# Kernel optimization log

Measured on AMD Instinct MI355X. Metric: run time of the kernel, lower is better.

Reference implementation:

```python
import jax, jax.numpy as jnp
import numpy as np

B, C, H, W = 16, 256, 32, 32
NUM_LAYERS = 30
OUT = 16  # sqrt(out_channels)
EPS = 1e-5


def setup_inputs() -> dict:
    key = jax.random.key(0)
    k1, k2, k3 = jax.random.split(key, 3)
    x = jax.random.normal(k1, (B, C, H, W), dtype=jnp.float32)
    # delta_t ~ small positive values (module inits ~N(0.01, 0.005))
    delta_t = jax.random.uniform(k2, (NUM_LAYERS, 1), dtype=jnp.float32) * 0.02
    matrices = jax.random.normal(k3, (NUM_LAYERS, 1, 1, OUT, OUT), dtype=jnp.float32) * 0.1
    gamma = jnp.ones((H * W,), dtype=jnp.float32)   # BatchNorm2d weight, oc = i*i = H*W
    beta = jnp.zeros((H * W,), dtype=jnp.float32)   # BatchNorm2d bias
    return {"x": x, "delta_t": delta_t, "matrices": matrices, "gamma": gamma, "beta": beta}


def _bn_relu6(z, gamma, beta):
    # training-mode BatchNorm2d over channel axis 1 (channels = H*W), then ReLU6
    mean = jnp.mean(z, axis=(0, 2, 3), keepdims=True)
    var = jnp.mean(jnp.square(z - mean), axis=(0, 2, 3), keepdims=True)  # biased var
    zhat = (z - mean) * jax.lax.rsqrt(var + EPS)
    g = gamma.reshape(1, -1, 1, 1)
    b = beta.reshape(1, -1, 1, 1)
    return jnp.clip(zhat * g + b, 0.0, 6.0)


def reference(x, delta_t, matrices, gamma, beta):
    b, c, h, w = x.shape
    hw = h * w
    # feature_reshape: [B,C,H,W] -> [B,HW,C] -> [B,HW,out,out] (inn == out branch)
    x1 = x.reshape(b, c, hw).transpose(0, 2, 1).reshape(b, hw, OUT, OUT)
    dt = jnp.clip(delta_t, 0.0, 6.0)[:, 0]  # relu6(delta_t), shape [L]

    def step(y0, params):
        m, dtl = params  # m: [1,1,out,out] broadcasts elementwise against x1
        dydt = -y0 + _bn_relu6(y0 + m * x1, gamma, beta)
        return y0 + dtl * dydt, None

    y0, _ = jax.lax.scan(step, x1, (matrices, dt))
    # (y0 + x1): [B, HW, out, out] -> view [B,H,W,out*out] -> permute to [B,out*out,H,W]
    y = (y0 + x1).reshape(b, h, w, OUT * OUT).transpose(0, 3, 1, 2)
    return y
```

## Files before the change

kernel.cpp:

```cpp
#include <hip/hip_runtime.h>

typedef float v2f __attribute__((ext_vector_type(2)));
typedef float v4f __attribute__((ext_vector_type(4)));

#define HW      1024
#define NROWS   4096
#define NLAYERS 30
#define TPB     256

static __device__ __forceinline__ v2f pk_fma(v2f a, v2f b, v2f c) {
    v2f d; asm("v_pk_fma_f32 %0, %1, %2, %3" : "=v"(d) : "v"(a), "v"(b), "v"(c));
    return d;
}
static __device__ __forceinline__ v2f pk_add(v2f a, v2f b) {
    v2f d; asm("v_pk_add_f32 %0, %1, %2" : "=v"(d) : "v"(a), "v"(b));
    return d;
}

template <int CTRL, int RMASK>
__device__ __forceinline__ float dpp_add(float x) {
    int t = __builtin_amdgcn_update_dpp(0, __builtin_bit_cast(int, x),
                                        CTRL, RMASK, 0xf, true);
    return x + __builtin_bit_cast(float, t);
}
__device__ __forceinline__ float wave_sum64(float x) {
    x = dpp_add<0x111, 0xf>(x);
    x = dpp_add<0x112, 0xf>(x);
    x = dpp_add<0x114, 0xf>(x);
    x = dpp_add<0x118, 0xf>(x);
    x = dpp_add<0x142, 0xa>(x);
    x = dpp_add<0x143, 0xc>(x);
    return x;
}
__device__ __forceinline__ float bcast63(float x) {
    return __builtin_bit_cast(float,
        __builtin_amdgcn_readlane(__builtin_bit_cast(int, x), 63));
}

__global__ __launch_bounds__(TPB) void txp64(const float* __restrict__ src,
                                             float* __restrict__ dst,
                                             int M, int N) {
    __shared__ float tile[64][65];
    const int n0 = blockIdx.x * 64;
    const int m0 = blockIdx.y * 64;
    const int tx = threadIdx.x & 63;
    const int ty = threadIdx.x >> 6;
#pragma unroll
    for (int i = 0; i < 16; ++i) {
        const int r = ty + 4 * i;
        tile[r][tx] = src[(size_t)(m0 + r) * N + n0 + tx];
    }
    __syncthreads();
#pragma unroll
    for (int i = 0; i < 16; ++i) {
        const int r = ty + 4 * i;
        dst[(size_t)(n0 + r) * M + m0 + tx] = tile[tx][r];
    }
}

__global__ __launch_bounds__(64, 1) void ode_zreg(
    float* __restrict__ ws, const float* __restrict__ delta_t,
    const float* __restrict__ matrices, const float* __restrict__ gamma,
    const float* __restrict__ beta) {

    const int p    = blockIdx.x;
    const int lane = threadIdx.x;
    const int c0   = 4 * lane;
    float* row = ws + (size_t)p * NROWS;

    const float gp = gamma[p];
    const float bp = beta[p];

    v4f xr[16];
    v2f z[32];
    v2f s0 = {0.f, 0.f}, s1 = {0.f, 0.f}, q0 = {0.f, 0.f}, q1 = {0.f, 0.f};

    {
        const v4f m4 = *(const v4f*)(matrices + c0);
        const v2f mA = {m4.x, m4.y}, mB = {m4.z, m4.w};
#pragma unroll
        for (int j = 0; j < 16; ++j) {
            xr[j] = *(const v4f*)(row + 4 * lane + 256 * j);
            const v2f xA = {xr[j].x, xr[j].y}, xB = {xr[j].z, xr[j].w};
            z[2 * j]     = pk_fma(mA, xA, xA);
            z[2 * j + 1] = pk_fma(mB, xB, xB);
            s0 = pk_add(s0, z[2 * j]);
            q0 = pk_fma(z[2 * j], z[2 * j], q0);
            s1 = pk_add(s1, z[2 * j + 1]);
            q1 = pk_fma(z[2 * j + 1], z[2 * j + 1], q1);
        }
    }

    v4f   mqc = *(const v4f*)(matrices + c0);
    v4f   mqn = *(const v4f*)(matrices + 256 + c0);
    float dtc = delta_t[0];
    float dtn = delta_t[1];

    for (int k = 0; k < NLAYERS - 1; ++k) {
        asm volatile("" : "+v"(xr[0]), "+v"(xr[1]), "+v"(xr[2]), "+v"(xr[3]));
        asm volatile("" : "+v"(xr[4]), "+v"(xr[5]), "+v"(xr[6]), "+v"(xr[7]));
        asm volatile("" : "+v"(xr[8]), "+v"(xr[9]), "+v"(xr[10]), "+v"(xr[11]));
        asm volatile("" : "+v"(xr[12]), "+v"(xr[13]), "+v"(xr[14]), "+v"(xr[15]));

        const int k2 = (k + 2 < NLAYERS) ? k + 2 : NLAYERS - 1;
        const v4f   mq2   = *(const v4f*)(matrices + k2 * 256 + c0);
        const float dt_nn = delta_t[k2];

        const v2f sv = pk_add(s0, s1);
        const v2f qv = pk_add(q0, q1);
        const float S = bcast63(wave_sum64(sv.x + sv.y));
        const float Q = bcast63(wave_sum64(qv.x + qv.y));

        const float dtk  = __builtin_amdgcn_fmed3f(dtc, 0.0f, 6.0f);
        const float mean = S * (1.0f / 4096.0f);
        const float var  = fmaf(-mean, mean, Q * (1.0f / 4096.0f));
        const float rstd = rsqrtf(var + 1e-5f);
        const float g    = gp * rstd;
        const float b    = fmaf(-mean, g, bp);
        const float om   = 1.0f - dtk;
        const float gd   = g * dtk;
        const float bd   = b * dtk;
        const float hi   = 6.0f * dtk;
        const v2f gd2 = {gd, gd}, bd2 = {bd, bd};
        const v2f om2 = {om, om};
        const v2f omn = {-om, -om};
        const v2f mcA = {mqc.x, mqc.y}, mcB = {mqc.z, mqc.w};
        const v2f mnA = {mqn.x, mqn.y}, mnB = {mqn.z, mqn.w};
        const v2f dmA = pk_fma(omn, mcA, mnA);
        const v2f dmB = pk_fma(omn, mcB, mnB);

        s0 = (v2f){0.f, 0.f}; s1 = (v2f){0.f, 0.f};
        q0 = (v2f){0.f, 0.f}; q1 = (v2f){0.f, 0.f};

#pragma unroll
        for (int j = 0; j < 16; ++j) {
            const v2f xA = {xr[j].x, xr[j].y}, xB = {xr[j].z, xr[j].w};
            {
                const int e = 2 * j;
                v2f a = pk_fma(z[e], gd2, bd2);
                a.x = __builtin_amdgcn_fmed3f(a.x, 0.0f, hi);
                a.y = __builtin_amdgcn_fmed3f(a.y, 0.0f, hi);
                v2f u = pk_fma(dmA, xA, a);
                z[e] = pk_fma(om2, z[e], u);
                s0 = pk_add(s0, z[e]);
                q0 = pk_fma(z[e], z[e], q0);
            }
            {
                const int e = 2 * j + 1;
                v2f a = pk_fma(z[e], gd2, bd2);
                a.x = __builtin_amdgcn_fmed3f(a.x, 0.0f, hi);
                a.y = __builtin_amdgcn_fmed3f(a.y, 0.0f, hi);
                v2f u = pk_fma(dmB, xB, a);
                z[e] = pk_fma(om2, z[e], u);
                s1 = pk_add(s1, z[e]);
                q1 = pk_fma(z[e], z[e], q1);
            }
        }

        mqc = mqn; mqn = mq2; dtc = dtn; dtn = dt_nn;
    }

    {
        const v2f sv = pk_add(s0, s1);
        const v2f qv = pk_add(q0, q1);
        const float S = bcast63(wave_sum64(sv.x + sv.y));
        const float Q = bcast63(wave_sum64(qv.x + qv.y));

        const float dtk  = __builtin_amdgcn_fmed3f(dtc, 0.0f, 6.0f);
        const float mean = S * (1.0f / 4096.0f);
        const float var  = fmaf(-mean, mean, Q * (1.0f / 4096.0f));
        const float rstd = rsqrtf(var + 1e-5f);
        const float g    = gp * rstd;
        const float b    = fmaf(-mean, g, bp);
        const float om   = 1.0f - dtk;
        const float gd   = g * dtk;
        const float bd   = b * dtk;
        const float hi   = 6.0f * dtk;
        const v2f gd2 = {gd, gd}, bd2 = {bd, bd};
        const v2f om2 = {om, om};
        const v2f omn = {-om, -om};
        const v2f one2 = {1.0f, 1.0f};
        const v2f mcA = {mqc.x, mqc.y}, mcB = {mqc.z, mqc.w};
        const v2f dmA = pk_fma(omn, mcA, one2);
        const v2f dmB = pk_fma(omn, mcB, one2);

#pragma unroll
        for (int j = 0; j < 16; ++j) {
            const v2f xA = {xr[j].x, xr[j].y}, xB = {xr[j].z, xr[j].w};
            v2f o0, o1;
            {
                v2f a = pk_fma(z[2 * j], gd2, bd2);
                a.x = __builtin_amdgcn_fmed3f(a.x, 0.0f, hi);
                a.y = __builtin_amdgcn_fmed3f(a.y, 0.0f, hi);
                v2f u = pk_fma(dmA, xA, a);
                o0 = pk_fma(om2, z[2 * j], u);
            }
            {
                v2f a = pk_fma(z[2 * j + 1], gd2, bd2);
                a.x = __builtin_amdgcn_fmed3f(a.x, 0.0f, hi);
                a.y = __builtin_amdgcn_fmed3f(a.y, 0.0f, hi);
                v2f u = pk_fma(dmB, xB, a);
                o1 = pk_fma(om2, z[2 * j + 1], u);
            }
            v4f o4; o4.x = o0.x; o4.y = o0.y; o4.z = o1.x; o4.w = o1.y;
            *(v4f*)(row + 4 * lane + 256 * j) = o4;
        }
    }
}

__global__ __launch_bounds__(TPB) void ode_fused(const float* __restrict__ x,
                                                 const float* __restrict__ delta_t,
                                                 const float* __restrict__ matrices,
                                                 const float* __restrict__ gamma,
                                                 const float* __restrict__ beta,
                                                 float* __restrict__ out) {
    const int bid = blockIdx.x;
    const int p   = ((bid & 7) << 7) | (bid >> 3);
    const int t   = threadIdx.x;

    __shared__ float smat[(NLAYERS + 1) * 256];
    __shared__ float sdt[NLAYERS];
    __shared__ __align__(16) v2f red[2][4];

#pragma unroll
    for (int i = 0; i < NLAYERS; ++i)
        smat[i * 256 + t] = matrices[i * 256 + t];
    if (t < NLAYERS)
        sdt[t] = __builtin_amdgcn_fmed3f(delta_t[t], 0.0f, 6.0f);

    v2f x1[8], y[8];
#pragma unroll
    for (int k = 0; k < 8; ++k) {
        x1[k].x = x[(size_t)(t + 512 * k) * HW + p];
        x1[k].y = x[(size_t)(t + 512 * k + 256) * HW + p];
        y[k] = x1[k];
    }

    const float gp   = gamma[p];
    const float bp   = beta[p];
    const int   wid  = t >> 6;
    const int   lane = t & 63;

    __syncthreads();
    float m_cur = smat[t];

    for (int l = 0; l < NLAYERS; ++l) {
        const float dtl = sdt[l];
        const v2f m2    = {m_cur, m_cur};
        const v2f dt2   = {dtl, dtl};
        const v2f om2   = {1.0f - dtl, 1.0f - dtl};

        v2f z[8];
        v2f sA = {0.f, 0.f}, sB = {0.f, 0.f};
        v2f qA = {0.f, 0.f}, qB = {0.f, 0.f};
#pragma unroll
        for (int k = 0; k < 8; k += 2) {
            z[k]     = __builtin_elementwise_fma(m2, x1[k], y[k]);
            z[k + 1] = __builtin_elementwise_fma(m2, x1[k + 1], y[k + 1]);
            sA += z[k];
            sB += z[k + 1];
            qA = __builtin_elementwise_fma(z[k], z[k], qA);
            qB = __builtin_elementwise_fma(z[k + 1], z[k + 1], qB);
        }
#pragma unroll
        for (int k = 0; k < 8; ++k) y[k] *= om2;

        const v2f sv = sA + sB;
        const v2f qv = qA + qB;
        float s = wave_sum64(sv.x + sv.y);
        float q = wave_sum64(qv.x + qv.y);

        const int par = l & 1;
        if (lane == 63) { v2f w; w.x = s; w.y = q; red[par][wid] = w; }
        m_cur = smat[(l + 1) * 256 + t];
        __syncthreads();

        const float4 r0 = *(const float4*)&red[par][0];
        const float4 r1 = *(const float4*)&red[par][2];
        const float S  = (r0.x + r0.z) + (r1.x + r1.z);
        const float S2 = (r0.y + r0.w) + (r1.y + r1.w);

        const float mean = S * (1.0f / 4096.0f);
        const float var  = fmaf(-mean, mean, S2 * (1.0f / 4096.0f));
        const float rstd = rsqrtf(var + 1e-5f);
        const float g    = gp * rstd;
        const float bb   = fmaf(-mean, g, bp);
        const v2f g2 = {g, g}, b2 = {bb, bb};
        const v2f z0 = {0.f, 0.f}, s6 = {6.f, 6.f};
#pragma unroll
        for (int k = 0; k < 8; ++k) {
            v2f a = __builtin_elementwise_fma(z[k], g2, b2);
            a = __builtin_elementwise_max(a, z0);
            a = __builtin_elementwise_min(a, s6);
            y[k] = __builtin_elementwise_fma(dt2, a, y[k]);
        }
    }

#pragma unroll
    for (int k = 0; k < 8; ++k) {
        out[(size_t)(t + 512 * k) * HW + p]       = y[k].x + x1[k].x;
        out[(size_t)(t + 512 * k + 256) * HW + p] = y[k].y + x1[k].y;
    }
}

extern "C" void kernel_launch(void* const* d_in, const int* in_sizes, int n_in,
                              void* d_out, int out_size, void* d_ws, size_t ws_size,
                              hipStream_t stream) {
    const float* x        = (const float*)d_in[0];
    const float* delta_t  = (const float*)d_in[1];
    const float* matrices = (const float*)d_in[2];
    const float* gamma    = (const float*)d_in[3];
    const float* beta     = (const float*)d_in[4];
    float* out = (float*)d_out;

    const size_t need = (size_t)HW * NROWS * sizeof(float);
    if (d_ws != nullptr && ws_size >= need) {
        float* ws = (float*)d_ws;
        txp64<<<dim3(HW / 64, NROWS / 64), dim3(TPB), 0, stream>>>(x, ws, NROWS, HW);
        ode_zreg<<<dim3(HW), dim3(64), 0, stream>>>(ws, delta_t, matrices, gamma, beta);
        txp64<<<dim3(NROWS / 64, HW / 64), dim3(TPB), 0, stream>>>(ws, out, HW, NROWS);
    } else {
        ode_fused<<<dim3(HW), dim3(TPB), 0, stream>>>(x, delta_t, matrices, gamma, beta, out);
    }
}
```

Baseline: 111.5 us.

## Fuse transposes into single-wave ODE kernel with strided direct global access

Removes the two transpose kernels and the workspace round trip, so the single-wave-per-column ODE kernel reads x and writes out directly with stride-HW scalar accesses. Blocks are remapped so that neighbouring blocks touch nearby columns, which lets cache lines be shared through L2. This drops two launches and a full extra read and write of the tensor. In exchange, every load and store is an uncoalesced 4-byte access, and a lot more memory transactions are issued. The ode_fused fallback is deleted.

Result: slower. 127.8 us (+14.6%).

```diff
diff --git a/kernel.cpp b/kernel.cpp
--- a/kernel.cpp
+++ b/kernel.cpp
@@ -6,7 +6,6 @@
 #define HW      1024
 #define NROWS   4096
 #define NLAYERS 30
-#define TPB     256
 
 static __device__ __forceinline__ v2f pk_fma(v2f a, v2f b, v2f c) {
     v2f d; asm("v_pk_fma_f32 %0, %1, %2, %3" : "=v"(d) : "v"(a), "v"(b), "v"(c));
@@ -37,39 +36,21 @@
         __builtin_amdgcn_readlane(__builtin_bit_cast(int, x), 63));
 }
 
-__global__ __launch_bounds__(TPB) void txp64(const float* __restrict__ src,
-                                             float* __restrict__ dst,
-                                             int M, int N) {
-    __shared__ float tile[64][65];
-    const int n0 = blockIdx.x * 64;
-    const int m0 = blockIdx.y * 64;
-    const int tx = threadIdx.x & 63;
-    const int ty = threadIdx.x >> 6;
-#pragma unroll
-    for (int i = 0; i < 16; ++i) {
-        const int r = ty + 4 * i;
-        tile[r][tx] = src[(size_t)(m0 + r) * N + n0 + tx];
-    }
-    __syncthreads();
-#pragma unroll
-    for (int i = 0; i < 16; ++i) {
-        const int r = ty + 4 * i;
-        dst[(size_t)(n0 + r) * M + m0 + tx] = tile[tx][r];
-    }
-}
-
-__global__ __launch_bounds__(64, 1) void ode_zreg(
-    float* __restrict__ ws, const float* __restrict__ delta_t,
+__global__ __launch_bounds__(64, 1) void ode_direct(
+    const float* __restrict__ x, const float* __restrict__ delta_t,
     const float* __restrict__ matrices, const float* __restrict__ gamma,
-    const float* __restrict__ beta) {
-
-    const int p    = blockIdx.x;
+    const float* __restrict__ beta, float* __restrict__ out) {
+
+    const int bid  = blockIdx.x;
+    const int p    = ((bid & 7) << 7) | (bid >> 3);
     const int lane = threadIdx.x;
     const int c0   = 4 * lane;
-    float* row = ws + (size_t)p * NROWS;
 
     const float gp = gamma[p];
     const float bp = beta[p];
+
+    const float* xp = x + (size_t)(4 * lane) * HW + p;
+    float*       op = out + (size_t)(4 * lane) * HW + p;
 
     v4f xr[16];
     v2f z[32];
@@ -80,8 +61,14 @@
         const v2f mA = {m4.x, m4.y}, mB = {m4.z, m4.w};
 #pragma unroll
         for (int j = 0; j < 16; ++j) {
-            xr[j] = *(const v4f*)(row + 4 * lane + 256 * j);
-            const v2f xA = {xr[j].x, xr[j].y}, xB = {xr[j].z, xr[j].w};
+            const size_t base = (size_t)(256 * j) * HW;
+            v4f v;
+            v.x = xp[base];
+            v.y = xp[base + HW];
+            v.z = xp[base + 2 * (size_t)HW];
+            v.w = xp[base + 3 * (size_t)HW];
+            xr[j] = v;
+            const v2f xA = {v.x, v.y}, xB = {v.z, v.w};
             z[2 * j]     = pk_fma(mA, xA, xA);
             z[2 * j + 1] = pk_fma(mB, xB, xB);
             s0 = pk_add(s0, z[2 * j]);
@@ -202,104 +189,12 @@
                 v2f u = pk_fma(dmB, xB, a);
                 o1 = pk_fma(om2, z[2 * j + 1], u);
             }
-            v4f o4; o4.x = o0.x; o4.y = o0.y; o4.z = o1.x; o4.w = o1.y;
-            *(v4f*)(row + 4 * lane + 256 * j) = o4;
+            const size_t base = (size_t)(256 * j) * HW;
+            op[base]                 = o0.x;
+            op[base + HW]            = o0.y;
+            op[base + 2 * (size_t)HW] = o1.x;
+            op[base + 3 * (size_t)HW] = o1.y;
         }
-    }
-}
-
-__global__ __launch_bounds__(TPB) void ode_fused(const float* __restrict__ x,
-                                                 const float* __restrict__ delta_t,
-                                                 const float* __restrict__ matrices,
-                                                 const float* __restrict__ gamma,
-                                                 const float* __restrict__ beta,
-                                                 float* __restrict__ out) {
-    const int bid = blockIdx.x;
-    const int p   = ((bid & 7) << 7) | (bid >> 3);
-    const int t   = threadIdx.x;
-
-    __shared__ float smat[(NLAYERS + 1) * 256];
-    __shared__ float sdt[NLAYERS];
-    __shared__ __align__(16) v2f red[2][4];
-
-#pragma unroll
-    for (int i = 0; i < NLAYERS; ++i)
-        smat[i * 256 + t] = matrices[i * 256 + t];
-    if (t < NLAYERS)
-        sdt[t] = __builtin_amdgcn_fmed3f(delta_t[t], 0.0f, 6.0f);
-
-    v2f x1[8], y[8];
-#pragma unroll
-    for (int k = 0; k < 8; ++k) {
-        x1[k].x = x[(size_t)(t + 512 * k) * HW + p];
-        x1[k].y = x[(size_t)(t + 512 * k + 256) * HW + p];
-        y[k] = x1[k];
-    }
-
-    const float gp   = gamma[p];
-    const float bp   = beta[p];
-    const int   wid  = t >> 6;
-    const int   lane = t & 63;
-
-    __syncthreads();
-    float m_cur = smat[t];
-
-    for (int l = 0; l < NLAYERS; ++l) {
-        const float dtl = sdt[l];
-        const v2f m2    = {m_cur, m_cur};
-        const v2f dt2   = {dtl, dtl};
-        const v2f om2   = {1.0f - dtl, 1.0f - dtl};
-
-        v2f z[8];
-        v2f sA = {0.f, 0.f}, sB = {0.f, 0.f};
-        v2f qA = {0.f, 0.f}, qB = {0.f, 0.f};
-#pragma unroll
-        for (int k = 0; k < 8; k += 2) {
-            z[k]     = __builtin_elementwise_fma(m2, x1[k], y[k]);
-            z[k + 1] = __builtin_elementwise_fma(m2, x1[k + 1], y[k + 1]);
-            sA += z[k];
-            sB += z[k + 1];
-            qA = __builtin_elementwise_fma(z[k], z[k], qA);
-            qB = __builtin_elementwise_fma(z[k + 1], z[k + 1], qB);
-        }
-#pragma unroll
-        for (int k = 0; k < 8; ++k) y[k] *= om2;
-
-        const v2f sv = sA + sB;
-        const v2f qv = qA + qB;
-        float s = wave_sum64(sv.x + sv.y);
-        float q = wave_sum64(qv.x + qv.y);
-
-        const int par = l & 1;
-        if (lane == 63) { v2f w; w.x = s; w.y = q; red[par][wid] = w; }
-        m_cur = smat[(l + 1) * 256 + t];
-        __syncthreads();
-
-        const float4 r0 = *(const float4*)&red[par][0];
-        const float4 r1 = *(const float4*)&red[par][2];
-        const float S  = (r0.x + r0.z) + (r1.x + r1.z);
-        const float S2 = (r0.y + r0.w) + (r1.y + r1.w);
-
-        const float mean = S * (1.0f / 4096.0f);
-        const float var  = fmaf(-mean, mean, S2 * (1.0f / 4096.0f));
-        const float rstd = rsqrtf(var + 1e-5f);
-        const float g    = gp * rstd;
-        const float bb   = fmaf(-mean, g, bp);
-        const v2f g2 = {g, g}, b2 = {bb, bb};
-        const v2f z0 = {0.f, 0.f}, s6 = {6.f, 6.f};
-#pragma unroll
-        for (int k = 0; k < 8; ++k) {
-            v2f a = __builtin_elementwise_fma(z[k], g2, b2);
-            a = __builtin_elementwise_max(a, z0);
-            a = __builtin_elementwise_min(a, s6);
-            y[k] = __builtin_elementwise_fma(dt2, a, y[k]);
-        }
-    }
-
-#pragma unroll
-    for (int k = 0; k < 8; ++k) {
-        out[(size_t)(t + 512 * k) * HW + p]       = y[k].x + x1[k].x;
-        out[(size_t)(t + 512 * k + 256) * HW + p] = y[k].y + x1[k].y;
     }
 }
 
@@ -313,13 +208,5 @@
     const float* beta     = (const float*)d_in[4];
     float* out = (float*)d_out;
 
-    const size_t need = (size_t)HW * NROWS * sizeof(float);
-    if (d_ws != nullptr && ws_size >= need) {
-        float* ws = (float*)d_ws;
-        txp64<<<dim3(HW / 64, NROWS / 64), dim3(TPB), 0, stream>>>(x, ws, NROWS, HW);
-        ode_zreg<<<dim3(HW), dim3(64), 0, stream>>>(ws, delta_t, matrices, gamma, beta);
-        txp64<<<dim3(NROWS / 64, HW / 64), dim3(TPB), 0, stream>>>(ws, out, HW, NROWS);
-    } else {
-        ode_fused<<<dim3(HW), dim3(TPB), 0, stream>>>(x, delta_t, matrices, gamma, beta, out);
-    }
-}
+    ode_direct<<<dim3(HW), dim3(64), 0, stream>>>(x, delta_t, matrices, gamma, beta, out);
+}
```

## Split each channel's ODE across two waves with LDS flag-based reduction

Applied to the files above, without the earlier changes.

Replaces the one-wave-per-channel ODE kernel with a two-wave (128-thread) block per channel. Each wave keeps half the elements in registers, and per-layer batch statistics are combined through shared-memory slots guarded by volatile tag spin-waits instead of a full barrier. This halves the serial per-wave work and register footprint so more waves can run concurrently, at the cost of an inter-wave handshake each layer. The final layer is folded into the loop behind a branch.

Measured after the change: 120.4 us. 8.0% more time.

```diff
diff --git a/kernel.cpp b/kernel.cpp
--- a/kernel.cpp
+++ b/kernel.cpp
@@ -32,10 +32,6 @@
     x = dpp_add<0x143, 0xc>(x);
     return x;
 }
-__device__ __forceinline__ float bcast63(float x) {
-    return __builtin_bit_cast(float,
-        __builtin_amdgcn_readlane(__builtin_bit_cast(int, x), 63));
-}
 
 __global__ __launch_bounds__(TPB) void txp64(const float* __restrict__ src,
                                              float* __restrict__ dst,
@@ -58,36 +54,46 @@
     }
 }
 
-__global__ __launch_bounds__(64, 1) void ode_zreg(
+__global__ __attribute__((amdgpu_waves_per_eu(2, 2)))
+__launch_bounds__(128) void ode_z2w(
     float* __restrict__ ws, const float* __restrict__ delta_t,
     const float* __restrict__ matrices, const float* __restrict__ gamma,
     const float* __restrict__ beta) {
 
     const int p    = blockIdx.x;
-    const int lane = threadIdx.x;
-    const int c0   = 4 * lane;
+    const int t    = threadIdx.x;
+    const int w    = t >> 6;
+    const int lane = t & 63;
+    const int c0   = (4 * t) & 255;
     float* row = ws + (size_t)p * NROWS;
+
+    __shared__ int   vtag[2][2];
+    __shared__ float vslt[2][2][2];
+    if (t < 4) ((int*)vtag)[t] = 0;
+    __syncthreads();
+
+    volatile int   (*tg)[2]    = (volatile int (*)[2])vtag;
+    volatile float (*sl)[2][2] = (volatile float (*)[2][2])vslt;
 
     const float gp = gamma[p];
     const float bp = beta[p];
 
-    v4f xr[16];
-    v2f z[32];
-    v2f s0 = {0.f, 0.f}, s1 = {0.f, 0.f}, q0 = {0.f, 0.f}, q1 = {0.f, 0.f};
+    v4f xr[8];
+    v2f z[16];
+    v2f s0 = {0.f, 0.f}, q0 = {0.f, 0.f};
 
     {
         const v4f m4 = *(const v4f*)(matrices + c0);
         const v2f mA = {m4.x, m4.y}, mB = {m4.z, m4.w};
 #pragma unroll
-        for (int j = 0; j < 16; ++j) {
-            xr[j] = *(const v4f*)(row + 4 * lane + 256 * j);
+        for (int j = 0; j < 8; ++j) {
+            xr[j] = *(const v4f*)(row + 4 * t + 512 * j);
             const v2f xA = {xr[j].x, xr[j].y}, xB = {xr[j].z, xr[j].w};
             z[2 * j]     = pk_fma(mA, xA, xA);
             z[2 * j + 1] = pk_fma(mB, xB, xB);
-            s0 = pk_add(s0, z[2 * j]);
+            s0 = pk_add(s0, pk_add(z[2 * j], z[2 * j + 1]));
             q0 = pk_fma(z[2 * j], z[2 * j], q0);
-            s1 = pk_add(s1, z[2 * j + 1]);
-            q1 = pk_fma(z[2 * j + 1], z[2 * j + 1], q1);
+            q0 = pk_fma(z[2 * j + 1], z[2 * j + 1], q0);
         }
     }
 
@@ -96,75 +102,27 @@
     float dtc = delta_t[0];
     float dtn = delta_t[1];
 
-    for (int k = 0; k < NLAYERS - 1; ++k) {
+    for (int k = 0; k < NLAYERS; ++k) {
         asm volatile("" : "+v"(xr[0]), "+v"(xr[1]), "+v"(xr[2]), "+v"(xr[3]));
         asm volatile("" : "+v"(xr[4]), "+v"(xr[5]), "+v"(xr[6]), "+v"(xr[7]));
-        asm volatile("" : "+v"(xr[8]), "+v"(xr[9]), "+v"(xr[10]), "+v"(xr[11]));
-        asm volatile("" : "+v"(xr[12]), "+v"(xr[13]), "+v"(xr[14]), "+v"(xr[15]));
 
         const int k2 = (k + 2 < NLAYERS) ? k + 2 : NLAYERS - 1;
         const v4f   mq2   = *(const v4f*)(matrices + k2 * 256 + c0);
         const float dt_nn = delta_t[k2];
 
-        const v2f sv = pk_add(s0, s1);
-        const v2f qv = pk_add(q0, q1);
-        const float S = bcast63(wave_sum64(sv.x + sv.y));
-        const float Q = bcast63(wave_sum64(qv.x + qv.y));
-
-        const float dtk  = __builtin_amdgcn_fmed3f(dtc, 0.0f, 6.0f);
-        const float mean = S * (1.0f / 4096.0f);
-        const float var  = fmaf(-mean, mean, Q * (1.0f / 4096.0f));
-        const float rstd = rsqrtf(var + 1e-5f);
-        const float g    = gp * rstd;
-        const float b    = fmaf(-mean, g, bp);
-        const float om   = 1.0f - dtk;
-        const float gd   = g * dtk;
-        const float bd   = b * dtk;
-        const float hi   = 6.0f * dtk;
-        const v2f gd2 = {gd, gd}, bd2 = {bd, bd};
-        const v2f om2 = {om, om};
-        const v2f omn = {-om, -om};
-        const v2f mcA = {mqc.x, mqc.y}, mcB = {mqc.z, mqc.w};
-        const v2f mnA = {mqn.x, mqn.y}, mnB = {mqn.z, mqn.w};
-        const v2f dmA = pk_fma(omn, mcA, mnA);
-        const v2f dmB = pk_fma(omn, mcB, mnB);
-
-        s0 = (v2f){0.f, 0.f}; s1 = (v2f){0.f, 0.f};
-        q0 = (v2f){0.f, 0.f}; q1 = (v2f){0.f, 0.f};
-
-#pragma unroll
-        for (int j = 0; j < 16; ++j) {
-            const v2f xA = {xr[j].x, xr[j].y}, xB = {xr[j].z, xr[j].w};
-            {
-                const int e = 2 * j;
-                v2f a = pk_fma(z[e], gd2, bd2);
-                a.x = __builtin_amdgcn_fmed3f(a.x, 0.0f, hi);
-                a.y = __builtin_amdgcn_fmed3f(a.y, 0.0f, hi);
-                v2f u = pk_fma(dmA, xA, a);
-                z[e] = pk_fma(om2, z[e], u);
-                s0 = pk_add(s0, z[e]);
-                q0 = pk_fma(z[e], z[e], q0);
-            }
-            {
-                const int e = 2 * j + 1;
-                v2f a = pk_fma(z[e], gd2, bd2);
-                a.x = __builtin_amdgcn_fmed3f(a.x, 0.0f, hi);
-                a.y = __builtin_amdgcn_fmed3f(a.y, 0.0f, hi);
-                v2f u = pk_fma(dmB, xB, a);
-                z[e] = pk_fma(om2, z[e], u);
-                s1 = pk_add(s1, z[e]);
-                q1 = pk_fma(z[e], z[e], q1);
-            }
-        }
-
-        mqc = mqn; mqn = mq2; dtc = dtn; dtn = dt_nn;
-    }
-
-    {
-        const v2f sv = pk_add(s0, s1);
-        const v2f qv = pk_add(q0, q1);
-        const float S = bcast63(wave_sum64(sv.x + sv.y));
-        const float Q = bcast63(wave_sum64(qv.x + qv.y));
+        const int   par  = k & 1;
+        const int   tagv = (k >> 1) + 1;
+        const float ss = wave_sum64(s0.x + s0.y);
+        const float qq = wave_sum64(q0.x + q0.y);
+        if (lane == 63) {
+            sl[par][w][0] = ss;
+            sl[par][w][1] = qq;
+            asm volatile("s_waitcnt lgkmcnt(0)" ::: "memory");
+            tg[par][w] = tagv;
+        }
+        while (tg[par][w ^ 1] < tagv) __builtin_amdgcn_s_sleep(1);
+        const float S = sl[par][0][0] + sl[par][1][0];
+        const float Q = sl[par][0][1] + sl[par][1][1];
 
         const float dtk  = __builtin_amdgcn_fmed3f(dtc, 0.0f, 6.0f);
         const float mean = S * (1.0f / 4096.0f);
@@ -181,30 +139,65 @@
         const v2f omn = {-om, -om};
         const v2f one2 = {1.0f, 1.0f};
         const v2f mcA = {mqc.x, mqc.y}, mcB = {mqc.z, mqc.w};
-        const v2f dmA = pk_fma(omn, mcA, one2);
-        const v2f dmB = pk_fma(omn, mcB, one2);
-
-#pragma unroll
-        for (int j = 0; j < 16; ++j) {
-            const v2f xA = {xr[j].x, xr[j].y}, xB = {xr[j].z, xr[j].w};
-            v2f o0, o1;
-            {
-                v2f a = pk_fma(z[2 * j], gd2, bd2);
-                a.x = __builtin_amdgcn_fmed3f(a.x, 0.0f, hi);
-                a.y = __builtin_amdgcn_fmed3f(a.y, 0.0f, hi);
-                v2f u = pk_fma(dmA, xA, a);
-                o0 = pk_fma(om2, z[2 * j], u);
+        const bool last = (k == NLAYERS - 1);
+        const v2f mnA = last ? one2 : (v2f){mqn.x, mqn.y};
+        const v2f mnB = last ? one2 : (v2f){mqn.z, mqn.w};
+        const v2f dmA = pk_fma(omn, mcA, mnA);
+        const v2f dmB = pk_fma(omn, mcB, mnB);
+
+        s0 = (v2f){0.f, 0.f};
+        q0 = (v2f){0.f, 0.f};
+
+        if (!last) {
+#pragma unroll
+            for (int j = 0; j < 8; ++j) {
+                const v2f xA = {xr[j].x, xr[j].y}, xB = {xr[j].z, xr[j].w};
+                {
+                    const int e = 2 * j;
+                    v2f a = pk_fma(z[e], gd2, bd2);
+                    a.x = __builtin_amdgcn_fmed3f(a.x, 0.0f, hi);
+                    a.y = __builtin_amdgcn_fmed3f(a.y, 0.0f, hi);
+                    v2f u = pk_fma(dmA, xA, a);
+                    z[e] = pk_fma(om2, z[e], u);
+                    s0 = pk_add(s0, z[e]);
+                    q0 = pk_fma(z[e], z[e], q0);
+                }
+                {
+                    const int e = 2 * j + 1;
+                    v2f a = pk_fma(z[e], gd2, bd2);
+                    a.x = __builtin_amdgcn_fmed3f(a.x, 0.0f, hi);
+                    a.y = __builtin_amdgcn_fmed3f(a.y, 0.0f, hi);
+                    v2f u = pk_fma(dmB, xB, a);
+                    z[e] = pk_fma(om2, z[e], u);
+                    s0 = pk_add(s0, z[e]);
+                    q0 = pk_fma(z[e], z[e], q0);
+                }
             }
-            {
-                v2f a = pk_fma(z[2 * j + 1], gd2, bd2);
-                a.x = __builtin_amdgcn_fmed3f(a.x, 0.0f, hi);
-                a.y = __builtin_amdgcn_fmed3f(a.y, 0.0f, hi);
-                v2f u = pk_fma(dmB, xB, a);
-                o1 = pk_fma(om2, z[2 * j + 1], u);
+        } else {
+#pragma unroll
+            for (int j = 0; j < 8; ++j) {
+                const v2f xA = {xr[j].x, xr[j].y}, xB = {xr[j].z, xr[j].w};
+                v2f o0, o1;
+                {
+                    v2f a = pk_fma(z[2 * j], gd2, bd2);
+                    a.x = __builtin_amdgcn_fmed3f(a.x, 0.0f, hi);
+                    a.y = __builtin_amdgcn_fmed3f(a.y, 0.0f, hi);
+                    v2f u = pk_fma(dmA, xA, a);
+                    o0 = pk_fma(om2, z[2 * j], u);
+                }
+                {
+                    v2f a = pk_fma(z[2 * j + 1], gd2, bd2);
+                    a.x = __builtin_amdgcn_fmed3f(a.x, 0.0f, hi);
+                    a.y = __builtin_amdgcn_fmed3f(a.y, 0.0f, hi);
+                    v2f u = pk_fma(dmB, xB, a);
+                    o1 = pk_fma(om2, z[2 * j + 1], u);
+                }
+                v4f o4; o4.x = o0.x; o4.y = o0.y; o4.z = o1.x; o4.w = o1.y;
+                *(v4f*)(row + 4 * t + 512 * j) = o4;
             }
-            v4f o4; o4.x = o0.x; o4.y = o0.y; o4.z = o1.x; o4.w = o1.y;
-            *(v4f*)(row + 4 * lane + 256 * j) = o4;
-        }
+        }
+
+        mqc = mqn; mqn = mq2; dtc = dtn; dtn = dt_nn;
     }
 }
 
@@ -271,7 +264,7 @@
         float q = wave_sum64(qv.x + qv.y);
 
         const int par = l & 1;
-        if (lane == 63) { v2f w; w.x = s; w.y = q; red[par][wid] = w; }
+        if (lane == 63) { v2f wv; wv.x = s; wv.y = q; red[par][wid] = wv; }
         m_cur = smat[(l + 1) * 256 + t];
         __syncthreads();
 
@@ -317,7 +310,7 @@
     if (d_ws != nullptr && ws_size >= need) {
         float* ws = (float*)d_ws;
         txp64<<<dim3(HW / 64, NROWS / 64), dim3(TPB), 0, stream>>>(x, ws, NROWS, HW);
-        ode_zreg<<<dim3(HW), dim3(64), 0, stream>>>(ws, delta_t, matrices, gamma, beta);
+        ode_z2w<<<dim3(HW), dim3(128), 0, stream>>>(ws, delta_t, matrices, gamma, beta);
         txp64<<<dim3(NROWS / 64, HW / 64), dim3(TPB), 0, stream>>>(ws, out, HW, NROWS);
     } else {
         ode_fused<<<dim3(HW), dim3(TPB), 0, stream>>>(x, delta_t, matrices, gamma, beta, out);
```
